# Performance work log

Hardware: AMD Instinct MI355X
Metric: run time of the kernel (lower is better)

Reference implementation:

```python
import jax, jax.numpy as jnp
import numpy as np

N_HEAD = 16

def setup_inputs() -> dict:
    key = jax.random.key(0)
    ks = jax.random.split(key, 8)
    B, S, D = 2, 2048, 1024
    s = 0.02
    return {
        "x": jax.random.normal(ks[0], (B, S, D), dtype=jnp.float32),
        "Wq": jax.random.normal(ks[1], (D, D), dtype=jnp.float32) * s,
        "bq": jax.random.normal(ks[2], (D,), dtype=jnp.float32) * s,
        "Wk": jax.random.normal(ks[3], (D, D), dtype=jnp.float32) * s,
        "Wv": jax.random.normal(ks[4], (D, D), dtype=jnp.float32) * s,
        "bv": jax.random.normal(ks[5], (D,), dtype=jnp.float32) * s,
        "Wo": jax.random.normal(ks[6], (D, D), dtype=jnp.float32) * s,
        "bo": jax.random.normal(ks[7], (D,), dtype=jnp.float32) * s,
    }

def reference(x, Wq, bq, Wk, Wv, bv, Wo, bo):
    B, S, D = x.shape
    H = N_HEAD
    dh = D // H
    scale = dh ** -0.25
    # projections (torch F.linear: x @ W.T + b)
    q = x @ Wq.T + bq
    k = x @ Wk.T              # key has no bias
    v = x @ Wv.T + bv
    # split heads: [B, H, S, dh]
    q = q.reshape(B, S, H, dh).transpose(0, 2, 1, 3) * scale
    k = k.reshape(B, S, H, dh).transpose(0, 2, 1, 3) * scale
    v = v.reshape(B, S, H, dh).transpose(0, 2, 1, 3)
    qk = jnp.einsum('bhqd,bhkd->bhqk', q, k)
    w = jax.nn.softmax(qk.astype(jnp.float32), axis=-1).astype(q.dtype)
    wv = jnp.einsum('bhqk,bhkd->bhqd', w, v)
    wv = wv.transpose(0, 2, 1, 3).reshape(B, S, D)
    out = wv @ Wo.T + bo
    return out, w
```

## Files before the change

### kernel.cpp

```cpp
#include <hip/hip_runtime.h>

typedef float  f32x4 __attribute__((ext_vector_type(4)));
typedef short  s16x8 __attribute__((ext_vector_type(8)));
typedef unsigned short u16x4 __attribute__((ext_vector_type(4)));


static __device__ __forceinline__ unsigned short f2bf(float f) {
  unsigned u = __builtin_bit_cast(unsigned, f);
  u += 0x7fffu + ((u >> 16) & 1u);
  return (unsigned short)(u >> 16);
}

static __device__ __forceinline__ void glds16(const void* g, void* l) {
  __builtin_amdgcn_global_load_lds(
      (const __attribute__((address_space(1))) unsigned int*)g,
      (__attribute__((address_space(3))) unsigned int*)l, 16, 0, 0);
}

static __device__ __forceinline__ void ntst4(float* p, f32x4 v) {
  __builtin_nontemporal_store(v, (f32x4*)p);
}

static __device__ __forceinline__ void stage64(const unsigned short* gsrc, int gstride,
                                               unsigned short* lbase, int wid, int lane) {
#pragma unroll
  for (int i = 0; i < 2; ++i) {
    int slotbase = (i * 4 + wid) * 64;
    int slot = slotbase + lane;
    int row = slot >> 3;
    int cs = (slot & 7) ^ (row & 7);
    glds16(&gsrc[(size_t)row * gstride + cs * 8], &lbase[slotbase * 8]);
  }
}

__global__ __launch_bounds__(256) void cvt_all(
    const float4* __restrict__ x,  const float4* __restrict__ wq,
    const float4* __restrict__ wk, const float4* __restrict__ wv,
    const float4* __restrict__ wo,
    u16x4* __restrict__ xb,  u16x4* __restrict__ wqb,
    u16x4* __restrict__ wkb, u16x4* __restrict__ wvb,
    u16x4* __restrict__ wob) {
  int b = blockIdx.x;
  const float4* s; u16x4* d; int o;
  if (b < 4096)      { s = x;  d = xb;  o = b; }
  else if (b < 5120) { s = wq; d = wqb; o = b - 4096; }
  else if (b < 6144) { s = wk; d = wkb; o = b - 5120; }
  else if (b < 7168) { s = wv; d = wvb; o = b - 6144; }
  else               { s = wo; d = wob; o = b - 7168; }
  int i = o * 256 + threadIdx.x;
  float4 v = s[i];
  u16x4 r = { f2bf(v.x), f2bf(v.y), f2bf(v.z), f2bf(v.w) };
  d[i] = r;
}

static __device__ __forceinline__ void gemm_body(
    int bid, unsigned short* at, unsigned short* bt,
    const unsigned short* __restrict__ A, const unsigned short* __restrict__ Bm,
    const float* __restrict__ bias, float scale, int mode, void* __restrict__ out) {
  const int tid = threadIdx.x, lane = tid & 63, wid = tid >> 6;
  const int l15 = lane & 15, l4 = lane >> 4;
  const int nb = (bid & 7) * 128, mb = (bid >> 3) * 128;
  const int wm = (wid >> 1) * 64, wn = (wid & 1) * 64;

  f32x4 acc[4][4];
#pragma unroll
  for (int mt = 0; mt < 4; ++mt)
#pragma unroll
    for (int nt = 0; nt < 4; ++nt) acc[mt][nt] = {0.f, 0.f, 0.f, 0.f};

  for (int k0 = 0; k0 < 1024; k0 += 64) {
#pragma unroll
    for (int i = 0; i < 4; ++i) {
      int slotbase = (i * 4 + wid) * 64;
      int slot = slotbase + lane;
      int row = slot >> 3;
      int cs = (slot & 7) ^ (row & 7);
      glds16(&A[(mb + row) * 1024 + k0 + cs * 8], &at[slotbase * 8]);
      glds16(&Bm[(nb + row) * 1024 + k0 + cs * 8], &bt[slotbase * 8]);
    }
    __syncthreads();
#pragma unroll
    for (int ks = 0; ks < 2; ++ks) {
      s16x8 af[4], bf[4];
#pragma unroll
      for (int mt = 0; mt < 4; ++mt) {
        int row = wm + mt * 16 + l15;
        af[mt] = *(const s16x8*)((const char*)&at[row * 64] +
                                 ((ks * 64 + l4 * 16) ^ ((row & 7) << 4)));
      }
#pragma unroll
      for (int nt = 0; nt < 4; ++nt) {
        int row = wn + nt * 16 + l15;
        bf[nt] = *(const s16x8*)((const char*)&bt[row * 64] +
                                 ((ks * 64 + l4 * 16) ^ ((row & 7) << 4)));
      }
#pragma unroll
      for (int mt = 0; mt < 4; ++mt)
#pragma unroll
        for (int nt = 0; nt < 4; ++nt)
          acc[mt][nt] = __builtin_amdgcn_mfma_f32_16x16x32_bf16(af[mt], bf[nt],
                                                                acc[mt][nt], 0, 0, 0);
    }
    __syncthreads();
  }

#pragma unroll
  for (int mt = 0; mt < 4; ++mt)
#pragma unroll
    for (int nt = 0; nt < 4; ++nt) {
      int n = nb + wn + nt * 16 + l15;
      float bvv = bias ? bias[n] : 0.0f;
      int m0 = mb + wm + mt * 16 + l4 * 4;
      if (mode == 0) {
#pragma unroll
        for (int r = 0; r < 4; ++r) {
          int m = m0 + r;
          float v = (acc[mt][nt][r] + bvv) * scale;
          int bb = m >> 11, s = m & 2047, hh = n >> 6, d = n & 63;
          ((unsigned short*)out)[(size_t)((bb * 16 + hh) * 2048 + s) * 64 + d] = f2bf(v);
        }
      } else if (mode == 1) {
        int bb = m0 >> 11, s0 = m0 & 2047, hh = n >> 6, d = n & 63;
        u16x4 p;
#pragma unroll
        for (int r = 0; r < 4; ++r) p[r] = f2bf(acc[mt][nt][r] + bvv);
        *(u16x4*)&((unsigned short*)out)[(size_t)((bb * 16 + hh) * 64 + d) * 2048 + s0] = p;
      } else {
#pragma unroll
        for (int r = 0; r < 4; ++r) {
          int m = m0 + r;
          ((float*)out)[(size_t)m * 1024 + n] = acc[mt][nt][r] + bvv;
        }
      }
    }
}

__global__ __launch_bounds__(256) void gemm_qkv(
    const unsigned short* __restrict__ xb,
    const unsigned short* __restrict__ Wqb, const unsigned short* __restrict__ Wkb,
    const unsigned short* __restrict__ Wvb,
    const float* __restrict__ bq, const float* __restrict__ bv,
    unsigned short* __restrict__ Qb, unsigned short* __restrict__ Kb,
    unsigned short* __restrict__ Vtb, float kscale) {
  __shared__ unsigned short at[128 * 64];
  __shared__ unsigned short bt[128 * 64];
  int sw = (blockIdx.x & 7) * 96 + (blockIdx.x >> 3);
  int op = sw >> 8, bid = sw & 255;
  if (op == 0)      gemm_body(bid, at, bt, xb, Wqb, bq,      kscale, 0, Qb);
  else if (op == 1) gemm_body(bid, at, bt, xb, Wkb, nullptr, kscale, 0, Kb);
  else              gemm_body(bid, at, bt, xb, Wvb, bv,      1.0f,   1, Vtb);
}

__global__ __launch_bounds__(256) void gemm_o(
    const unsigned short* __restrict__ A, const unsigned short* __restrict__ Wob,
    const float* __restrict__ bo, float* __restrict__ out) {
  __shared__ unsigned short at[128 * 64];
  __shared__ unsigned short bt[128 * 64];
  int sw = (blockIdx.x & 7) * 32 + (blockIdx.x >> 3);
  gemm_body(sw, at, bt, A, Wob, bo, 1.0f, 2, out);
}

__global__ __launch_bounds__(256) void attn_sumexp(const unsigned short* __restrict__ Q,
                                                   const unsigned short* __restrict__ K,
                                                   float* __restrict__ lsum) {
  __shared__ unsigned short kt[2][64 * 64];
  const int tid = threadIdx.x, lane = tid & 63, wid = tid >> 6;
  const int l15 = lane & 15, l4 = lane >> 4;
  const int sw = (blockIdx.x & 7) * 64 + (blockIdx.x >> 3);
  const int bh = sw >> 4;
  const int qb = (sw & 15) * 128;
  const int q0 = qb + wid * 32 + l15;

  s16x8 qf[2][2];
#pragma unroll
  for (int qg = 0; qg < 2; ++qg)
#pragma unroll
    for (int t = 0; t < 2; ++t)
      qf[qg][t] = *(const s16x8*)&Q[(size_t)(bh * 2048 + q0 + qg * 16) * 64 + t * 32 + l4 * 8];

  float acc0 = 0.f, acc1 = 0.f;
  const unsigned short* Kbh = &K[(size_t)bh * 2048 * 64];

  stage64(&Kbh[0], 64, &kt[0][0], wid, lane);
  int cur = 0;
  for (int t = 0; t < 32; ++t) {
    if (t < 31) {
      stage64(&Kbh[(size_t)(t + 1) * 64 * 64], 64, &kt[cur ^ 1][0], wid, lane);
      asm volatile("s_waitcnt vmcnt(2)" ::: "memory");
    } else {
      asm volatile("s_waitcnt vmcnt(0)" ::: "memory");
    }
    __builtin_amdgcn_sched_barrier(0);
    __builtin_amdgcn_s_barrier();
#pragma unroll
    for (int ks = 0; ks < 4; ++ks) {
      int row = ks * 16 + l15;
      const char* rbase = (const char*)&kt[cur][row * 64];
      s16x8 a0 = *(const s16x8*)(rbase + ((l4 * 16) ^ ((row & 7) << 4)));
      s16x8 a1 = *(const s16x8*)(rbase + ((64 + l4 * 16) ^ ((row & 7) << 4)));
      f32x4 c0 = {0.f, 0.f, 0.f, 0.f}, c1 = {0.f, 0.f, 0.f, 0.f};
      c0 = __builtin_amdgcn_mfma_f32_16x16x32_bf16(a0, qf[0][0], c0, 0, 0, 0);
      c0 = __builtin_amdgcn_mfma_f32_16x16x32_bf16(a1, qf[0][1], c0, 0, 0, 0);
      c1 = __builtin_amdgcn_mfma_f32_16x16x32_bf16(a0, qf[1][0], c1, 0, 0, 0);
      c1 = __builtin_amdgcn_mfma_f32_16x16x32_bf16(a1, qf[1][1], c1, 0, 0, 0);
      acc0 += __expf(c0[0]) + __expf(c0[1]) + __expf(c0[2]) + __expf(c0[3]);
      acc1 += __expf(c1[0]) + __expf(c1[1]) + __expf(c1[2]) + __expf(c1[3]);
    }
    __builtin_amdgcn_s_barrier();
    cur ^= 1;
  }
  acc0 += __shfl_xor(acc0, 16); acc0 += __shfl_xor(acc0, 32);
  acc1 += __shfl_xor(acc1, 16); acc1 += __shfl_xor(acc1, 32);
  if (l4 == 0) {
    lsum[bh * 2048 + q0] = acc0;
    lsum[bh * 2048 + q0 + 16] = acc1;
  }
}

__global__ __launch_bounds__(256) void attn_wv(const unsigned short* __restrict__ Q,
                                               const unsigned short* __restrict__ K,
                                               const unsigned short* __restrict__ Vt,
                                               const float* __restrict__ lsum,
                                               float* __restrict__ wout,
                                               unsigned short* __restrict__ wv) {
  __shared__ unsigned short kt[2][64 * 64];
  __shared__ unsigned short vt[2][64 * 64];
  __shared__ unsigned short pt[4][2][16 * 64];
  const int tid = threadIdx.x, lane = tid & 63, wid = tid >> 6;
  const int l15 = lane & 15, l4 = lane >> 4;
  const int sw = (blockIdx.x & 7) * 64 + (blockIdx.x >> 3);
  const int bh = sw >> 4;
  const int qb = (sw & 15) * 128;
  const int q0 = qb + wid * 32 + l15;

  s16x8 qf[2][2];
#pragma unroll
  for (int qg = 0; qg < 2; ++qg)
#pragma unroll
    for (int t = 0; t < 2; ++t)
      qf[qg][t] = *(const s16x8*)&Q[(size_t)(bh * 2048 + q0 + qg * 16) * 64 + t * 32 + l4 * 8];
  float rcpl0 = 1.0f / lsum[bh * 2048 + q0];
  float rcpl1 = 1.0f / lsum[bh * 2048 + q0 + 16];
  float* wrow0 = &wout[((size_t)bh * 2048 + q0) * 2048];
  float* wrow1 = wrow0 + (size_t)16 * 2048;

  f32x4 oacc[2][4];
#pragma unroll
  for (int qg = 0; qg < 2; ++qg)
#pragma unroll
    for (int dt = 0; dt < 4; ++dt) oacc[qg][dt] = {0.f, 0.f, 0.f, 0.f};

  const unsigned short* Kbh = &K[(size_t)bh * 2048 * 64];
  const unsigned short* Vbh = &Vt[(size_t)bh * 64 * 2048];

  stage64(&Kbh[0], 64, &kt[0][0], wid, lane);
  stage64(&Vbh[0], 2048, &vt[0][0], wid, lane);
  int cur = 0;
  for (int t = 0; t < 32; ++t) {
    int k0 = t * 64;
    if (t < 31) {
      stage64(&Kbh[(size_t)(t + 1) * 64 * 64], 64, &kt[cur ^ 1][0], wid, lane);
      stage64(&Vbh[k0 + 64], 2048, &vt[cur ^ 1][0], wid, lane);
      asm volatile("s_waitcnt vmcnt(4)" ::: "memory");
    } else {
      asm volatile("s_waitcnt vmcnt(0)" ::: "memory");
    }
    __builtin_amdgcn_sched_barrier(0);
    __builtin_amdgcn_s_barrier();

#pragma unroll
    for (int ks = 0; ks < 4; ++ks) {
      int row = ks * 16 + l15;
      const char* rbase = (const char*)&kt[cur][row * 64];
      s16x8 a0 = *(const s16x8*)(rbase + ((l4 * 16) ^ ((row & 7) << 4)));
      s16x8 a1 = *(const s16x8*)(rbase + ((64 + l4 * 16) ^ ((row & 7) << 4)));
      f32x4 c0 = {0.f, 0.f, 0.f, 0.f}, c1 = {0.f, 0.f, 0.f, 0.f};
      c0 = __builtin_amdgcn_mfma_f32_16x16x32_bf16(a0, qf[0][0], c0, 0, 0, 0);
      c0 = __builtin_amdgcn_mfma_f32_16x16x32_bf16(a1, qf[0][1], c0, 0, 0, 0);
      c1 = __builtin_amdgcn_mfma_f32_16x16x32_bf16(a0, qf[1][0], c1, 0, 0, 0);
      c1 = __builtin_amdgcn_mfma_f32_16x16x32_bf16(a1, qf[1][1], c1, 0, 0, 0);
      float w00 = __expf(c0[0]) * rcpl0, w01 = __expf(c0[1]) * rcpl0;
      float w02 = __expf(c0[2]) * rcpl0, w03 = __expf(c0[3]) * rcpl0;
      float w10 = __expf(c1[0]) * rcpl1, w11 = __expf(c1[1]) * rcpl1;
      float w12 = __expf(c1[2]) * rcpl1, w13 = __expf(c1[3]) * rcpl1;
      ntst4(&wrow0[k0 + ks * 16 + l4 * 4], (f32x4){w00, w01, w02, w03});
      ntst4(&wrow1[k0 + ks * 16 + l4 * 4], (f32x4){w10, w11, w12, w13});
      u16x4 pb0 = {f2bf(w00), f2bf(w01), f2bf(w02), f2bf(w03)};
      u16x4 pb1 = {f2bf(w10), f2bf(w11), f2bf(w12), f2bf(w13)};
      *(u16x4*)((char*)&pt[wid][0][l15 * 64] + ((ks * 32 + l4 * 8) ^ ((l15 & 7) << 4))) = pb0;
      *(u16x4*)((char*)&pt[wid][1][l15 * 64] + ((ks * 32 + l4 * 8) ^ ((l15 & 7) << 4))) = pb1;
    }
#pragma unroll
    for (int t2 = 0; t2 < 2; ++t2) {
      s16x8 pa0 = *(const s16x8*)((char*)&pt[wid][0][l15 * 64] +
                                  ((t2 * 64 + l4 * 16) ^ ((l15 & 7) << 4)));
      s16x8 pa1 = *(const s16x8*)((char*)&pt[wid][1][l15 * 64] +
                                  ((t2 * 64 + l4 * 16) ^ ((l15 & 7) << 4)));
#pragma unroll
      for (int dt = 0; dt < 4; ++dt) {
        int vrow = dt * 16 + l15;
        s16x8 vb = *(const s16x8*)((const char*)&vt[cur][vrow * 64] +
                                   ((t2 * 64 + l4 * 16) ^ ((vrow & 7) << 4)));
        oacc[0][dt] = __builtin_amdgcn_mfma_f32_16x16x32_bf16(pa0, vb, oacc[0][dt], 0, 0, 0);
        oacc[1][dt] = __builtin_amdgcn_mfma_f32_16x16x32_bf16(pa1, vb, oacc[1][dt], 0, 0, 0);
      }
    }
    __builtin_amdgcn_s_barrier();
    cur ^= 1;
  }
  int b = bh >> 4, h = bh & 15;
#pragma unroll
  for (int qg = 0; qg < 2; ++qg)
#pragma unroll
    for (int dt = 0; dt < 4; ++dt)
#pragma unroll
      for (int r = 0; r < 4; ++r) {
        int sq = qb + wid * 32 + qg * 16 + l4 * 4 + r;
        int d = dt * 16 + l15;
        wv[(size_t)(b * 2048 + sq) * 1024 + h * 64 + d] = f2bf(oacc[qg][dt][r]);
      }
}

extern "C" void kernel_launch(void* const* d_in, const int* in_sizes, int n_in,
                              void* d_out, int out_size, void* d_ws, size_t ws_size,
                              hipStream_t stream) {
  const float* x  = (const float*)d_in[0];
  const float* Wq = (const float*)d_in[1];
  const float* bq = (const float*)d_in[2];
  const float* Wk = (const float*)d_in[3];
  const float* Wv = (const float*)d_in[4];
  const float* bv = (const float*)d_in[5];
  const float* Wo = (const float*)d_in[6];
  const float* bo = (const float*)d_in[7];
  float* out  = (float*)d_out;
  float* wout = out + 4194304;

  unsigned short* xb  = (unsigned short*)d_ws;
  unsigned short* Wqb = xb + 4194304;
  unsigned short* Wkb = Wqb + 1048576;
  unsigned short* Wvb = Wkb + 1048576;
  unsigned short* Wob = Wvb + 1048576;
  unsigned short* Qb  = Wob + 1048576;
  unsigned short* Kb  = Qb + 4194304;
  unsigned short* Vtb = Kb + 4194304;
  float* lsum = (float*)(Vtb + 4194304);
  unsigned short* wvb = xb;

  cvt_all<<<8192, 256, 0, stream>>>((const float4*)x, (const float4*)Wq,
                                    (const float4*)Wk, (const float4*)Wv,
                                    (const float4*)Wo,
                                    (u16x4*)xb, (u16x4*)Wqb, (u16x4*)Wkb,
                                    (u16x4*)Wvb, (u16x4*)Wob);

  const float kscale = 0.35355339059327373f;
  gemm_qkv<<<768, 256, 0, stream>>>(xb, Wqb, Wkb, Wvb, bq, bv, Qb, Kb, Vtb, kscale);

  attn_sumexp<<<512, 256, 0, stream>>>(Qb, Kb, lsum);
  attn_wv<<<512, 256, 0, stream>>>(Qb, Kb, Vtb, lsum, wout, wvb);

  gemm_o<<<256, 256, 0, stream>>>(wvb, Wob, bo, out);
}
```

Measured before the change: 760.0 us.

## Double-buffer GEMMs, fuse attention passes, triple-buffer K/V, retile output GEMM

The QKV and output GEMMs now double-buffer their LDS tiles, so the next K-slice is loaded while MFMAs run on the current one. The two attention kernels (sum-exp pass and weighted-V pass) are merged into one, which removes a launch and the lsum round trip through global memory. K/V staging in attention is deepened to three buffers with adjusted waitcnt values. The output GEMM uses 128x64 tiles to launch 512 blocks for better CU occupancy. The cost is more LDS per block, which may reduce occupancy.

```diff
diff --git a/kernel.cpp b/kernel.cpp
--- a/kernel.cpp
+++ b/kernel.cpp
@@ -21,15 +21,16 @@
   __builtin_nontemporal_store(v, (f32x4*)p);
 }
 
-static __device__ __forceinline__ void stage64(const unsigned short* gsrc, int gstride,
-                                               unsigned short* lbase, int wid, int lane) {
-#pragma unroll
-  for (int i = 0; i < 2; ++i) {
+template <int R>
+static __device__ __forceinline__ void stage_rows(const unsigned short* g, int gstride,
+                                                  unsigned short* l, int wid, int lane) {
+#pragma unroll
+  for (int i = 0; i < R / 32; ++i) {
     int slotbase = (i * 4 + wid) * 64;
     int slot = slotbase + lane;
     int row = slot >> 3;
     int cs = (slot & 7) ^ (row & 7);
-    glds16(&gsrc[(size_t)row * gstride + cs * 8], &lbase[slotbase * 8]);
+    glds16(&g[(size_t)row * gstride + cs * 8], &l[slotbase * 8]);
   }
 }
 
@@ -53,88 +54,6 @@
   d[i] = r;
 }
 
-static __device__ __forceinline__ void gemm_body(
-    int bid, unsigned short* at, unsigned short* bt,
-    const unsigned short* __restrict__ A, const unsigned short* __restrict__ Bm,
-    const float* __restrict__ bias, float scale, int mode, void* __restrict__ out) {
-  const int tid = threadIdx.x, lane = tid & 63, wid = tid >> 6;
-  const int l15 = lane & 15, l4 = lane >> 4;
-  const int nb = (bid & 7) * 128, mb = (bid >> 3) * 128;
-  const int wm = (wid >> 1) * 64, wn = (wid & 1) * 64;
-
-  f32x4 acc[4][4];
-#pragma unroll
-  for (int mt = 0; mt < 4; ++mt)
-#pragma unroll
-    for (int nt = 0; nt < 4; ++nt) acc[mt][nt] = {0.f, 0.f, 0.f, 0.f};
-
-  for (int k0 = 0; k0 < 1024; k0 += 64) {
-#pragma unroll
-    for (int i = 0; i < 4; ++i) {
-      int slotbase = (i * 4 + wid) * 64;
-      int slot = slotbase + lane;
-      int row = slot >> 3;
-      int cs = (slot & 7) ^ (row & 7);
-      glds16(&A[(mb + row) * 1024 + k0 + cs * 8], &at[slotbase * 8]);
-      glds16(&Bm[(nb + row) * 1024 + k0 + cs * 8], &bt[slotbase * 8]);
-    }
-    __syncthreads();
-#pragma unroll
-    for (int ks = 0; ks < 2; ++ks) {
-      s16x8 af[4], bf[4];
-#pragma unroll
-      for (int mt = 0; mt < 4; ++mt) {
-        int row = wm + mt * 16 + l15;
-        af[mt] = *(const s16x8*)((const char*)&at[row * 64] +
-                                 ((ks * 64 + l4 * 16) ^ ((row & 7) << 4)));
-      }
-#pragma unroll
-      for (int nt = 0; nt < 4; ++nt) {
-        int row = wn + nt * 16 + l15;
-        bf[nt] = *(const s16x8*)((const char*)&bt[row * 64] +
-                                 ((ks * 64 + l4 * 16) ^ ((row & 7) << 4)));
-      }
-#pragma unroll
-      for (int mt = 0; mt < 4; ++mt)
-#pragma unroll
-        for (int nt = 0; nt < 4; ++nt)
-          acc[mt][nt] = __builtin_amdgcn_mfma_f32_16x16x32_bf16(af[mt], bf[nt],
-                                                                acc[mt][nt], 0, 0, 0);
-    }
-    __syncthreads();
-  }
-
-#pragma unroll
-  for (int mt = 0; mt < 4; ++mt)
-#pragma unroll
-    for (int nt = 0; nt < 4; ++nt) {
-      int n = nb + wn + nt * 16 + l15;
-      float bvv = bias ? bias[n] : 0.0f;
-      int m0 = mb + wm + mt * 16 + l4 * 4;
-      if (mode == 0) {
-#pragma unroll
-        for (int r = 0; r < 4; ++r) {
-          int m = m0 + r;
-          float v = (acc[mt][nt][r] + bvv) * scale;
-          int bb = m >> 11, s = m & 2047, hh = n >> 6, d = n & 63;
-          ((unsigned short*)out)[(size_t)((bb * 16 + hh) * 2048 + s) * 64 + d] = f2bf(v);
-        }
-      } else if (mode == 1) {
-        int bb = m0 >> 11, s0 = m0 & 2047, hh = n >> 6, d = n & 63;
-        u16x4 p;
-#pragma unroll
-        for (int r = 0; r < 4; ++r) p[r] = f2bf(acc[mt][nt][r] + bvv);
-        *(u16x4*)&((unsigned short*)out)[(size_t)((bb * 16 + hh) * 64 + d) * 2048 + s0] = p;
-      } else {
-#pragma unroll
-        for (int r = 0; r < 4; ++r) {
-          int m = m0 + r;
-          ((float*)out)[(size_t)m * 1024 + n] = acc[mt][nt][r] + bvv;
-        }
-      }
-    }
-}
-
 __global__ __launch_bounds__(256) void gemm_qkv(
     const unsigned short* __restrict__ xb,
     const unsigned short* __restrict__ Wqb, const unsigned short* __restrict__ Wkb,
@@ -142,28 +61,175 @@
     const float* __restrict__ bq, const float* __restrict__ bv,
     unsigned short* __restrict__ Qb, unsigned short* __restrict__ Kb,
     unsigned short* __restrict__ Vtb, float kscale) {
-  __shared__ unsigned short at[128 * 64];
-  __shared__ unsigned short bt[128 * 64];
+  __shared__ unsigned short at[2][128 * 64];
+  __shared__ unsigned short bt[2][128 * 64];
+  const int tid = threadIdx.x, lane = tid & 63, wid = tid >> 6;
+  const int l15 = lane & 15, l4 = lane >> 4;
   int sw = (blockIdx.x & 7) * 96 + (blockIdx.x >> 3);
   int op = sw >> 8, bid = sw & 255;
-  if (op == 0)      gemm_body(bid, at, bt, xb, Wqb, bq,      kscale, 0, Qb);
-  else if (op == 1) gemm_body(bid, at, bt, xb, Wkb, nullptr, kscale, 0, Kb);
-  else              gemm_body(bid, at, bt, xb, Wvb, bv,      1.0f,   1, Vtb);
+  const unsigned short* A = xb;
+  const unsigned short* Bm; const float* bias; float scale; int mode;
+  void* outp;
+  if (op == 0)      { Bm = Wqb; bias = bq;      scale = kscale; mode = 0; outp = Qb; }
+  else if (op == 1) { Bm = Wkb; bias = nullptr; scale = kscale; mode = 0; outp = Kb; }
+  else              { Bm = Wvb; bias = bv;      scale = 1.0f;   mode = 1; outp = Vtb; }
+
+  const int nb = (bid & 7) * 128, mb = (bid >> 3) * 128;
+  const int wm = (wid >> 1) * 64, wn = (wid & 1) * 64;
+
+  f32x4 acc[4][4];
+#pragma unroll
+  for (int mt = 0; mt < 4; ++mt)
+#pragma unroll
+    for (int nt = 0; nt < 4; ++nt) acc[mt][nt] = {0.f, 0.f, 0.f, 0.f};
+
+  stage_rows<128>(&A[(size_t)mb * 1024], 1024, at[0], wid, lane);
+  stage_rows<128>(&Bm[(size_t)nb * 1024], 1024, bt[0], wid, lane);
+  asm volatile("s_waitcnt vmcnt(0)" ::: "memory");
+  __builtin_amdgcn_sched_barrier(0);
+  __builtin_amdgcn_s_barrier();
+
+  int cur = 0;
+  for (int t = 0; t < 16; ++t) {
+    if (t < 15) {
+      stage_rows<128>(&A[(size_t)mb * 1024 + (t + 1) * 64], 1024, at[cur ^ 1], wid, lane);
+      stage_rows<128>(&Bm[(size_t)nb * 1024 + (t + 1) * 64], 1024, bt[cur ^ 1], wid, lane);
+    }
+#pragma unroll
+    for (int ks = 0; ks < 2; ++ks) {
+      s16x8 af[4], bf[4];
+#pragma unroll
+      for (int mt = 0; mt < 4; ++mt) {
+        int row = wm + mt * 16 + l15;
+        af[mt] = *(const s16x8*)((const char*)&at[cur][row * 64] +
+                                 ((ks * 64 + l4 * 16) ^ ((row & 7) << 4)));
+      }
+#pragma unroll
+      for (int nt = 0; nt < 4; ++nt) {
+        int row = wn + nt * 16 + l15;
+        bf[nt] = *(const s16x8*)((const char*)&bt[cur][row * 64] +
+                                 ((ks * 64 + l4 * 16) ^ ((row & 7) << 4)));
+      }
+#pragma unroll
+      for (int mt = 0; mt < 4; ++mt)
+#pragma unroll
+        for (int nt = 0; nt < 4; ++nt)
+          acc[mt][nt] = __builtin_amdgcn_mfma_f32_16x16x32_bf16(af[mt], bf[nt],
+                                                                acc[mt][nt], 0, 0, 0);
+    }
+    if (t < 15) {
+      asm volatile("s_waitcnt vmcnt(0)" ::: "memory");
+      __builtin_amdgcn_sched_barrier(0);
+      __builtin_amdgcn_s_barrier();
+      cur ^= 1;
+    }
+  }
+
+#pragma unroll
+  for (int mt = 0; mt < 4; ++mt)
+#pragma unroll
+    for (int nt = 0; nt < 4; ++nt) {
+      int n = nb + wn + nt * 16 + l15;
+      float bvv = bias ? bias[n] : 0.0f;
+      int m0 = mb + wm + mt * 16 + l4 * 4;
+      if (mode == 0) {
+#pragma unroll
+        for (int r = 0; r < 4; ++r) {
+          int m = m0 + r;
+          float v = (acc[mt][nt][r] + bvv) * scale;
+          int bb = m >> 11, s = m & 2047, hh = n >> 6, d = n & 63;
+          ((unsigned short*)outp)[(size_t)((bb * 16 + hh) * 2048 + s) * 64 + d] = f2bf(v);
+        }
+      } else {
+        int bb = m0 >> 11, s0 = m0 & 2047, hh = n >> 6, d = n & 63;
+        u16x4 p;
+#pragma unroll
+        for (int r = 0; r < 4; ++r) p[r] = f2bf(acc[mt][nt][r] + bvv);
+        *(u16x4*)&((unsigned short*)outp)[(size_t)((bb * 16 + hh) * 64 + d) * 2048 + s0] = p;
+      }
+    }
 }
 
 __global__ __launch_bounds__(256) void gemm_o(
     const unsigned short* __restrict__ A, const unsigned short* __restrict__ Wob,
     const float* __restrict__ bo, float* __restrict__ out) {
-  __shared__ unsigned short at[128 * 64];
-  __shared__ unsigned short bt[128 * 64];
-  int sw = (blockIdx.x & 7) * 32 + (blockIdx.x >> 3);
-  gemm_body(sw, at, bt, A, Wob, bo, 1.0f, 2, out);
-}
-
-__global__ __launch_bounds__(256) void attn_sumexp(const unsigned short* __restrict__ Q,
-                                                   const unsigned short* __restrict__ K,
-                                                   float* __restrict__ lsum) {
-  __shared__ unsigned short kt[2][64 * 64];
+  __shared__ unsigned short at[2][128 * 64];
+  __shared__ unsigned short bt[2][64 * 64];
+  const int tid = threadIdx.x, lane = tid & 63, wid = tid >> 6;
+  const int l15 = lane & 15, l4 = lane >> 4;
+  int sw = (blockIdx.x & 7) * 64 + (blockIdx.x >> 3);
+  const int nb = (sw & 15) * 64, mb = (sw >> 4) * 128;
+  const int wm = (wid >> 1) * 64, wn = (wid & 1) * 32;
+
+  f32x4 acc[4][2];
+#pragma unroll
+  for (int mt = 0; mt < 4; ++mt)
+#pragma unroll
+    for (int nt = 0; nt < 2; ++nt) acc[mt][nt] = {0.f, 0.f, 0.f, 0.f};
+
+  stage_rows<128>(&A[(size_t)mb * 1024], 1024, at[0], wid, lane);
+  stage_rows<64>(&Wob[(size_t)nb * 1024], 1024, bt[0], wid, lane);
+  asm volatile("s_waitcnt vmcnt(0)" ::: "memory");
+  __builtin_amdgcn_sched_barrier(0);
+  __builtin_amdgcn_s_barrier();
+
+  int cur = 0;
+  for (int t = 0; t < 16; ++t) {
+    if (t < 15) {
+      stage_rows<128>(&A[(size_t)mb * 1024 + (t + 1) * 64], 1024, at[cur ^ 1], wid, lane);
+      stage_rows<64>(&Wob[(size_t)nb * 1024 + (t + 1) * 64], 1024, bt[cur ^ 1], wid, lane);
+    }
+#pragma unroll
+    for (int ks = 0; ks < 2; ++ks) {
+      s16x8 af[4], bf[2];
+#pragma unroll
+      for (int mt = 0; mt < 4; ++mt) {
+        int row = wm + mt * 16 + l15;
+        af[mt] = *(const s16x8*)((const char*)&at[cur][row * 64] +
+                                 ((ks * 64 + l4 * 16) ^ ((row & 7) << 4)));
+      }
+#pragma unroll
+      for (int nt = 0; nt < 2; ++nt) {
+        int row = wn + nt * 16 + l15;
+        bf[nt] = *(const s16x8*)((const char*)&bt[cur][row * 64] +
+                                 ((ks * 64 + l4 * 16) ^ ((row & 7) << 4)));
+      }
+#pragma unroll
+      for (int mt = 0; mt < 4; ++mt)
+#pragma unroll
+        for (int nt = 0; nt < 2; ++nt)
+          acc[mt][nt] = __builtin_amdgcn_mfma_f32_16x16x32_bf16(af[mt], bf[nt],
+                                                                acc[mt][nt], 0, 0, 0);
+    }
+    if (t < 15) {
+      asm volatile("s_waitcnt vmcnt(0)" ::: "memory");
+      __builtin_amdgcn_sched_barrier(0);
+      __builtin_amdgcn_s_barrier();
+      cur ^= 1;
+    }
+  }
+
+#pragma unroll
+  for (int mt = 0; mt < 4; ++mt)
+#pragma unroll
+    for (int nt = 0; nt < 2; ++nt) {
+      int n = nb + wn + nt * 16 + l15;
+      float bvv = bo[n];
+      int m0 = mb + wm + mt * 16 + l4 * 4;
+#pragma unroll
+      for (int r = 0; r < 4; ++r)
+        out[(size_t)(m0 + r) * 1024 + n] = acc[mt][nt][r] + bvv;
+    }
+}
+
+__global__ __launch_bounds__(256) void attn_fused(const unsigned short* __restrict__ Q,
+                                                  const unsigned short* __restrict__ K,
+                                                  const unsigned short* __restrict__ Vt,
+                                                  float* __restrict__ wout,
+                                                  unsigned short* __restrict__ wv) {
+  __shared__ unsigned short kt[3][64 * 64];
+  __shared__ unsigned short vt[3][64 * 64];
+  __shared__ unsigned short pt[4][2][16 * 64];
   const int tid = threadIdx.x, lane = tid & 63, wid = tid >> 6;
   const int l15 = lane & 15, l4 = lane >> 4;
   const int sw = (blockIdx.x & 7) * 64 + (blockIdx.x >> 3);
@@ -178,24 +244,28 @@
     for (int t = 0; t < 2; ++t)
       qf[qg][t] = *(const s16x8*)&Q[(size_t)(bh * 2048 + q0 + qg * 16) * 64 + t * 32 + l4 * 8];
 
+  const unsigned short* Kbh = &K[(size_t)bh * 2048 * 64];
+  const unsigned short* Vbh = &Vt[(size_t)bh * 64 * 2048];
+
   float acc0 = 0.f, acc1 = 0.f;
-  const unsigned short* Kbh = &K[(size_t)bh * 2048 * 64];
-
-  stage64(&Kbh[0], 64, &kt[0][0], wid, lane);
-  int cur = 0;
+  stage_rows<64>(&Kbh[0], 64, kt[0], wid, lane);
+  stage_rows<64>(&Kbh[64 * 64], 64, kt[1], wid, lane);
   for (int t = 0; t < 32; ++t) {
-    if (t < 31) {
-      stage64(&Kbh[(size_t)(t + 1) * 64 * 64], 64, &kt[cur ^ 1][0], wid, lane);
+    if (t < 30) {
+      stage_rows<64>(&Kbh[(size_t)(t + 2) * 64 * 64], 64, kt[(t + 2) % 3], wid, lane);
+      asm volatile("s_waitcnt vmcnt(4)" ::: "memory");
+    } else if (t == 30) {
       asm volatile("s_waitcnt vmcnt(2)" ::: "memory");
     } else {
       asm volatile("s_waitcnt vmcnt(0)" ::: "memory");
     }
     __builtin_amdgcn_sched_barrier(0);
     __builtin_amdgcn_s_barrier();
+    const unsigned short* kcur = kt[t % 3];
 #pragma unroll
     for (int ks = 0; ks < 4; ++ks) {
       int row = ks * 16 + l15;
-      const char* rbase = (const char*)&kt[cur][row * 64];
+      const char* rbase = (const char*)&kcur[row * 64];
       s16x8 a0 = *(const s16x8*)(rbase + ((l4 * 16) ^ ((row & 7) << 4)));
       s16x8 a1 = *(const s16x8*)(rbase + ((64 + l4 * 16) ^ ((row & 7) << 4)));
       f32x4 c0 = {0.f, 0.f, 0.f, 0.f}, c1 = {0.f, 0.f, 0.f, 0.f};
@@ -207,40 +277,10 @@
       acc1 += __expf(c1[0]) + __expf(c1[1]) + __expf(c1[2]) + __expf(c1[3]);
     }
     __builtin_amdgcn_s_barrier();
-    cur ^= 1;
   }
   acc0 += __shfl_xor(acc0, 16); acc0 += __shfl_xor(acc0, 32);
   acc1 += __shfl_xor(acc1, 16); acc1 += __shfl_xor(acc1, 32);
-  if (l4 == 0) {
-    lsum[bh * 2048 + q0] = acc0;
-    lsum[bh * 2048 + q0 + 16] = acc1;
-  }
-}
-
-__global__ __launch_bounds__(256) void attn_wv(const unsigned short* __restrict__ Q,
-                                               const unsigned short* __restrict__ K,
-                                               const unsigned short* __restrict__ Vt,
-                                               const float* __restrict__ lsum,
-                                               float* __restrict__ wout,
-                                               unsigned short* __restrict__ wv) {
-  __shared__ unsigned short kt[2][64 * 64];
-  __shared__ unsigned short vt[2][64 * 64];
-  __shared__ unsigned short pt[4][2][16 * 64];
-  const int tid = threadIdx.x, lane = tid & 63, wid = tid >> 6;
-  const int l15 = lane & 15, l4 = lane >> 4;
-  const int sw = (blockIdx.x & 7) * 64 + (blockIdx.x >> 3);
-  const int bh = sw >> 4;
-  const int qb = (sw & 15) * 128;
-  const int q0 = qb + wid * 32 + l15;
-
-  s16x8 qf[2][2];
-#pragma unroll
-  for (int qg = 0; qg < 2; ++qg)
-#pragma unroll
-    for (int t = 0; t < 2; ++t)
-      qf[qg][t] = *(const s16x8*)&Q[(size_t)(bh * 2048 + q0 + qg * 16) * 64 + t * 32 + l4 * 8];
-  float rcpl0 = 1.0f / lsum[bh * 2048 + q0];
-  float rcpl1 = 1.0f / lsum[bh * 2048 + q0 + 16];
+  float rcpl0 = 1.0f / acc0, rcpl1 = 1.0f / acc1;
   float* wrow0 = &wout[((size_t)bh * 2048 + q0) * 2048];
   float* wrow1 = wrow0 + (size_t)16 * 2048;
 
@@ -250,28 +290,30 @@
 #pragma unroll
     for (int dt = 0; dt < 4; ++dt) oacc[qg][dt] = {0.f, 0.f, 0.f, 0.f};
 
-  const unsigned short* Kbh = &K[(size_t)bh * 2048 * 64];
-  const unsigned short* Vbh = &Vt[(size_t)bh * 64 * 2048];
-
-  stage64(&Kbh[0], 64, &kt[0][0], wid, lane);
-  stage64(&Vbh[0], 2048, &vt[0][0], wid, lane);
-  int cur = 0;
+  stage_rows<64>(&Kbh[0], 64, kt[0], wid, lane);
+  stage_rows<64>(&Vbh[0], 2048, vt[0], wid, lane);
+  stage_rows<64>(&Kbh[64 * 64], 64, kt[1], wid, lane);
+  stage_rows<64>(&Vbh[64], 2048, vt[1], wid, lane);
   for (int t = 0; t < 32; ++t) {
     int k0 = t * 64;
-    if (t < 31) {
-      stage64(&Kbh[(size_t)(t + 1) * 64 * 64], 64, &kt[cur ^ 1][0], wid, lane);
-      stage64(&Vbh[k0 + 64], 2048, &vt[cur ^ 1][0], wid, lane);
+    if (t < 30) {
+      stage_rows<64>(&Kbh[(size_t)(t + 2) * 64 * 64], 64, kt[(t + 2) % 3], wid, lane);
+      stage_rows<64>(&Vbh[k0 + 128], 2048, vt[(t + 2) % 3], wid, lane);
+      asm volatile("s_waitcnt vmcnt(8)" ::: "memory");
+    } else if (t == 30) {
       asm volatile("s_waitcnt vmcnt(4)" ::: "memory");
     } else {
       asm volatile("s_waitcnt vmcnt(0)" ::: "memory");
     }
     __builtin_amdgcn_sched_barrier(0);
     __builtin_amdgcn_s_barrier();
+    const unsigned short* kcur = kt[t % 3];
+    const unsigned short* vcur = vt[t % 3];
 
 #pragma unroll
     for (int ks = 0; ks < 4; ++ks) {
       int row = ks * 16 + l15;
-      const char* rbase = (const char*)&kt[cur][row * 64];
+      const char* rbase = (const char*)&kcur[row * 64];
       s16x8 a0 = *(const s16x8*)(rbase + ((l4 * 16) ^ ((row & 7) << 4)));
       s16x8 a1 = *(const s16x8*)(rbase + ((64 + l4 * 16) ^ ((row & 7) << 4)));
       f32x4 c0 = {0.f, 0.f, 0.f, 0.f}, c1 = {0.f, 0.f, 0.f, 0.f};
@@ -299,14 +341,13 @@
 #pragma unroll
       for (int dt = 0; dt < 4; ++dt) {
         int vrow = dt * 16 + l15;
-        s16x8 vb = *(const s16x8*)((const char*)&vt[cur][vrow * 64] +
+        s16x8 vb = *(const s16x8*)((const char*)&vcur[vrow * 64] +
                                    ((t2 * 64 + l4 * 16) ^ ((vrow & 7) << 4)));
         oacc[0][dt] = __builtin_amdgcn_mfma_f32_16x16x32_bf16(pa0, vb, oacc[0][dt], 0, 0, 0);
         oacc[1][dt] = __builtin_amdgcn_mfma_f32_16x16x32_bf16(pa1, vb, oacc[1][dt], 0, 0, 0);
       }
     }
     __builtin_amdgcn_s_barrier();
-    cur ^= 1;
   }
   int b = bh >> 4, h = bh & 15;
 #pragma unroll
@@ -343,7 +384,6 @@
   unsigned short* Qb  = Wob + 1048576;
   unsigned short* Kb  = Qb + 4194304;
   unsigned short* Vtb = Kb + 4194304;
-  float* lsum = (float*)(Vtb + 4194304);
   unsigned short* wvb = xb;
 
   cvt_all<<<8192, 256, 0, stream>>>((const float4*)x, (const float4*)Wq,
@@ -355,8 +395,7 @@
   const float kscale = 0.35355339059327373f;
   gemm_qkv<<<768, 256, 0, stream>>>(xb, Wqb, Wkb, Wvb, bq, bv, Qb, Kb, Vtb, kscale);
 
-  attn_sumexp<<<512, 256, 0, stream>>>(Qb, Kb, lsum);
-  attn_wv<<<512, 256, 0, stream>>>(Qb, Kb, Vtb, lsum, wout, wvb);
-
-  gemm_o<<<256, 256, 0, stream>>>(wvb, Wob, bo, out);
-}
+  attn_fused<<<512, 256, 0, stream>>>(Qb, Kb, Vtb, wout, wvb);
+
+  gemm_o<<<512, 256, 0, stream>>>(wvb, Wob, bo, out);
+}
```

Result: no change. 758.8 us (-0.2%).
